# Optimization experiments

Measured on AMD Instinct MI355X. Metric: run time of the kernel, lower is better.

The kernel has to match this reference:

```python
import jax, jax.numpy as jnp
import numpy as np

B, T, N, D, INTER, KS = 8, 12, 325, 64, 16, 3
BN_EPS = 1e-5
LN_EPS = 1e-5


def _stx(x):
    # [B,T,N,D] -> edge-pad time, unfold window 3 -> [B,T,3N,D] (window-major like torch reshape)
    xp = jnp.concatenate([x[:, :1], x, x[:, -1:]], axis=1)          # [B,T+2,N,D]
    w = jnp.stack([xp[:, i:i + T] for i in range(3)], axis=2)        # [B,T,3,N,D]
    return w.reshape(x.shape[0], T, 3 * N, x.shape[-1])


def _conv1x1(y, W, b):
    # y: [B,C,T,N], W: [O,C], b: [O]
    return jnp.einsum('bctn,oc->botn', y, W) + b[None, :, None, None]


def _bn_eval(y, g, b):
    # BatchNorm2d eval with running mean 0 / var 1
    return y * (g / jnp.sqrt(1.0 + BN_EPS))[None, :, None, None] + b[None, :, None, None]


def setup_inputs() -> dict:
    key = jax.random.key(0)
    ks = jax.random.split(key, 32)
    inp = {}
    inp['x'] = jax.random.normal(ks[0], (B, T, N, D), jnp.float32)
    inp['gso'] = jax.random.normal(ks[1], (B, N, N), jnp.float32) * 0.05
    inp['geo_mask'] = jax.random.bernoulli(ks[2], 0.5, (N, N))
    s = 1.0 / np.sqrt(D)
    inp['Wq'] = jax.random.normal(ks[3], (D, D), jnp.float32) * s
    inp['Wk'] = jax.random.normal(ks[4], (D, D), jnp.float32) * s
    inp['Wv'] = jax.random.normal(ks[5], (D, D), jnp.float32) * s
    inp['cheb_w'] = jax.random.normal(ks[6], (KS, D, D), jnp.float32) * s
    inp['p_t12'] = jax.random.normal(ks[7], (N,), jnp.float32)
    inp['p_t21'] = jax.random.normal(ks[8], (N,), jnp.float32)
    inp['p_t23'] = jax.random.normal(ks[9], (N,), jnp.float32)
    inp['p_t32'] = jax.random.normal(ks[10], (N,), jnp.float32)
    inp['ln_g'] = jnp.ones((D,), jnp.float32)
    inp['ln_b'] = jnp.zeros((D,), jnp.float32)
    si = 1.0 / np.sqrt(INTER)
    for pfx, kk in (('l', 11), ('g', 17)):
        inp[pfx + '_w1'] = jax.random.normal(ks[kk], (INTER, D), jnp.float32) * s
        inp[pfx + '_b1'] = jax.random.normal(ks[kk + 1], (INTER,), jnp.float32) * s
        inp[pfx + '_g1'] = jnp.ones((INTER,), jnp.float32)
        inp[pfx + '_be1'] = jnp.zeros((INTER,), jnp.float32)
        inp[pfx + '_w2'] = jax.random.normal(ks[kk + 2], (D, INTER), jnp.float32) * si
        inp[pfx + '_b2'] = jax.random.normal(ks[kk + 3], (D,), jnp.float32) * si
        inp[pfx + '_g2'] = jnp.ones((D,), jnp.float32)
        inp[pfx + '_be2'] = jnp.zeros((D,), jnp.float32)
    return inp


def _forward(x, gso, geo_mask, Wq, Wk, Wv, cheb_w, p_t12, p_t21, p_t23, p_t32,
             ln_g, ln_b,
             l_w1, l_b1, l_g1, l_be1, l_w2, l_b2, l_g2, l_be2,
             g_w1, g_b1, g_g1, g_be1, g_w2, g_b2, g_g2, g_be2):
    M = 3 * N
    stX = _stx(x)                                                    # [B,T,M,D]

    # ---- DSTFormer: masked spatiotemporal attention (no scaling, per source) ----
    q = jnp.einsum('btmd,od->btmo', stX, Wq)
    k = jnp.einsum('btmd,od->btmo', stX, Wk)
    v = jnp.einsum('btmd,od->btmo', stX, Wv)
    attn = jnp.einsum('btmo,btno->btmn', q, k)                       # [B,T,M,M]
    eye = jnp.eye(N, dtype=bool)
    uneye = ~eye
    tru = jnp.ones((N, N), dtype=bool)
    big_mask = jnp.block([[geo_mask, uneye, tru],
                          [uneye, geo_mask, uneye],
                          [tru, uneye, geo_mask]])                   # [M,M]
    attn = jnp.where(big_mask, -jnp.inf, attn)
    p = jax.nn.softmax(attn, axis=-1)
    sem = jnp.einsum('btmn,btno->btmo', p, v)                        # [B,T,M,D]
    # faithful to torch: transpose(2,3) then reshape(B,T,M,-1) (mixes layout)
    y = jnp.swapaxes(sem, 2, 3).reshape(B, T, M, D)
    attn_out = y.reshape(B, T, 3, N, D)[:, :, 1]                     # [B,T,N,D]

    # ---- DSTGCN: Chebyshev conv on assembled [B,3N,3N] shift operator ----
    Z = jnp.zeros((B, N, N), x.dtype)
    dg = lambda vv: jnp.broadcast_to(jnp.diag(vv), (B, N, N))
    row0 = jnp.concatenate([gso, dg(p_t21), Z], axis=2)
    row1 = jnp.concatenate([dg(p_t12), gso, dg(p_t32)], axis=2)
    row2 = jnp.concatenate([Z, dg(p_t23), gso], axis=2)
    L = jnp.concatenate([row0, row1, row2], axis=1)                  # [B,M,M]
    xs = [stX, jnp.einsum('bhi,btij->bthj', L, stX)]
    for kk in range(2, KS):
        xs.append(jnp.einsum('bhi,btij->bthj', 2.0 * L, xs[kk - 1]) - xs[kk - 2])
    xk = jnp.stack(xs, axis=2)                                       # [B,T,KS,M,D]
    h = jnp.einsum('btkhi,kij->bthj', xk, cheb_w)                    # [B,T,M,D]
    h = jnp.transpose(h, (0, 3, 1, 2)).reshape(B, D, T, 3, N)[:, :, :, 1, :]  # [B,D,T,N]
    h = jnp.transpose(h, (0, 2, 3, 1))                               # [B,T,N,D]
    mu = h.mean(-1, keepdims=True)
    var = ((h - mu) ** 2).mean(-1, keepdims=True)
    gcn_out = (h - mu) / jnp.sqrt(var + LN_EPS) * ln_g + ln_b

    # ---- AFF fusion on channel-first maps ----
    xc = jnp.transpose(attn_out, (0, 3, 1, 2))                       # [B,D,T,N]
    rc = jnp.transpose(gcn_out, (0, 3, 1, 2))
    xa = xc + rc
    zl = jax.nn.relu(_bn_eval(_conv1x1(xa, l_w1, l_b1), l_g1, l_be1))
    xl = _bn_eval(_conv1x1(zl, l_w2, l_b2), l_g2, l_be2)
    m = xa.mean((2, 3), keepdims=True)
    zg = jax.nn.relu(_bn_eval(_conv1x1(m, g_w1, g_b1), g_g1, g_be1))
    xg = _bn_eval(_conv1x1(zg, g_w2, g_b2), g_g2, g_be2)
    wei = jax.nn.sigmoid(xl + xg)
    out = 2.0 * xc * wei + 2.0 * rc * (1.0 - wei)
    return jnp.transpose(out, (0, 2, 3, 1))                          # [B,T,N,D]


def reference(x, gso, geo_mask, Wq, Wk, Wv, cheb_w, p_t12, p_t21, p_t23, p_t32,
              ln_g, ln_b,
              l_w1, l_b1, l_g1, l_be1, l_w2, l_b2, l_g2, l_be2,
              g_w1, g_b1, g_g1, g_be1, g_w2, g_b2, g_g2, g_be2):
    return _forward(x, gso, geo_mask, Wq, Wk, Wv, cheb_w, p_t12, p_t21, p_t23, p_t32,
                    ln_g, ln_b,
                    l_w1, l_b1, l_g1, l_be1, l_w2, l_b2, l_g2, l_be2,
                    g_w1, g_b1, g_g1, g_be1, g_w2, g_b2, g_g2, g_be2)
```

## Files before the change

### kernel.cpp

```cpp
#include <hip/hip_runtime.h>
#include <math.h>

constexpr int TT = 12;
constexpr int NN = 325;
constexpr int MM = 975;
constexpr int DD = 64;
constexpr long SZ = 96L * MM * DD;
constexpr int GSTR = 352;
constexpr int MBSTR = 48;
constexpr int VTS = 22528;
constexpr float BN_EPS_ = 1e-5f;
constexpr float LN_EPS_ = 1e-5f;

constexpr long WS_MASKB = 0;
constexpr long WS_GSOB  = WS_MASKB + 4096;
constexpr long WS_STXB  = WS_GSOB + 457600;
constexpr long WS_QB    = WS_STXB + SZ / 2;
constexpr long WS_KB    = WS_QB + SZ / 2;
constexpr long WS_VB    = WS_KB + SZ / 2;
constexpr long WS_VT    = WS_VB + SZ / 2;
constexpr long WS_SEMH  = WS_VT + 3244032;
constexpr long WS_T2B   = WS_SEMH + SZ / 2;
constexpr long WS_MBD   = WS_T2B + 998400;

typedef _Float16 half8 __attribute__((ext_vector_type(8)));
typedef __attribute__((ext_vector_type(4))) float f32x4;

static __device__ inline unsigned short f2h(float f) {
  _Float16 h = (_Float16)f;
  return __builtin_bit_cast(unsigned short, h);
}
static __device__ inline float h2f(unsigned short s) {
  return (float)__builtin_bit_cast(_Float16, s);
}

__global__ __launch_bounds__(256) void k_maskprep(const unsigned char* __restrict__ raw,
                                                  unsigned char* __restrict__ outm) {
  bool is_u8 = false;
  for (int i = 0; i < 256; ++i) {
    if (raw[4 * i + 1]) { is_u8 = true; break; }
  }
  int idx = blockIdx.x * 256 + threadIdx.x;
  if (idx >= NN * MBSTR) return;
  int n = idx / MBSTR, jb = idx - n * MBSTR;
  unsigned char v = 0;
  for (int k = 0; k < 8; ++k) {
    int col = jb * 8 + k;
    bool m = true;
    if (col < NN) {
      int f = n * NN + col;
      m = is_u8 ? (raw[f] != 0) : (((const int*)raw)[f] != 0);
    }
    v |= (unsigned char)(m ? 1 : 0) << k;
  }
  outm[idx] = v;
}

__global__ __launch_bounds__(256) void k_gsoprep(const float* __restrict__ gso,
                                                 unsigned short* __restrict__ gsoB) {
  int idx = blockIdx.x * 256 + threadIdx.x;
  int b = idx / (NN * GSTR);
  int rem = idx - b * (NN * GSTR);
  int r = rem / GSTR, j = rem - r * GSTR;
  gsoB[idx] = (j < NN) ? f2h(gso[(long)b * NN * NN + r * NN + j]) : (unsigned short)0;
}

__global__ __launch_bounds__(256) void k_stx(const float* __restrict__ x,
                                             unsigned short* __restrict__ stXb) {
  int idx = blockIdx.x * 256 + threadIdx.x;
  int d = idx & 63;
  int m = (idx >> 6) % MM;
  int bt = idx / (MM * DD);
  int b = bt / TT, t = bt - b * TT;
  int w = m / NN, n = m - w * NN;
  int st = t + w - 1;
  st = st < 0 ? 0 : (st > TT - 1 ? TT - 1 : st);
  stXb[idx] = f2h(x[(((b * TT + st) * NN + n) << 6) + d]);
}

__global__ __launch_bounds__(256) void k_qkv_mfma(const unsigned short* __restrict__ stXb,
                                                  const float* __restrict__ Wq,
                                                  const float* __restrict__ Wk,
                                                  const float* __restrict__ Wv,
                                                  unsigned short* __restrict__ qb,
                                                  unsigned short* __restrict__ kb,
                                                  unsigned short* __restrict__ vb) {
  __shared__ alignas(16) unsigned short sX[128 * 72];
  __shared__ alignas(16) unsigned short sW[64 * 72];
  const float* W = blockIdx.y == 0 ? Wq : (blockIdx.y == 1 ? Wk : Wv);
  unsigned short* outb = blockIdx.y == 0 ? qb : (blockIdx.y == 1 ? kb : vb);
  int tid = threadIdx.x;
  long r0 = (long)blockIdx.x * 128;
  for (int u = 0; u < 4; ++u) {
    int idx = tid + 256 * u;
    int row = idx >> 3, c8 = idx & 7;
    long rg = r0 + row; if (rg > 93599) rg = 93599;
    *(uint4*)&sX[row * 72 + c8 * 8] = *(const uint4*)&stXb[rg * 64 + c8 * 8];
  }
  for (int u = 0; u < 16; ++u) {
    int f = tid + 256 * u;
    int o = f >> 6, d = f & 63;
    sW[o * 72 + d] = f2h(W[f]);
  }
  __syncthreads();
  int lane = tid & 63;
  int wv = __builtin_amdgcn_readfirstlane(tid >> 6);
  int lr = lane & 15, lg = lane >> 4;
  f32x4 zero4 = {0.f, 0.f, 0.f, 0.f};
  f32x4 acc[2][4];
#pragma unroll
  for (int rt = 0; rt < 2; ++rt)
#pragma unroll
    for (int c = 0; c < 4; ++c) acc[rt][c] = zero4;
#pragma unroll
  for (int kk = 0; kk < 2; ++kk) {
    half8 a0 = *(const half8*)&sX[(32 * wv + lr) * 72 + kk * 32 + lg * 8];
    half8 a1 = *(const half8*)&sX[(32 * wv + 16 + lr) * 72 + kk * 32 + lg * 8];
#pragma unroll
    for (int c = 0; c < 4; ++c) {
      half8 b = *(const half8*)&sW[(16 * c + lr) * 72 + kk * 32 + lg * 8];
      acc[0][c] = __builtin_amdgcn_mfma_f32_16x16x32_f16(a0, b, acc[0][c], 0, 0, 0);
      acc[1][c] = __builtin_amdgcn_mfma_f32_16x16x32_f16(a1, b, acc[1][c], 0, 0, 0);
    }
  }
  __syncthreads();
#pragma unroll
  for (int rt = 0; rt < 2; ++rt)
#pragma unroll
    for (int c = 0; c < 4; ++c)
#pragma unroll
      for (int e = 0; e < 4; ++e) {
        int row = 32 * wv + 16 * rt + lg * 4 + e;
        int col = 16 * c + lr;
        sX[row * 64 + col] = f2h(acc[rt][c][e]);
      }
  __syncthreads();
  for (int u = 0; u < 4; ++u) {
    int idx = tid + 256 * u;
    int row = idx >> 3, c8 = idx & 7;
    long rg = r0 + row;
    if (rg < 93600)
      *(uint4*)&outb[rg * 64 + c8 * 8] = *(const uint4*)&sX[row * 64 + c8 * 8];
  }
}

__global__ __launch_bounds__(256) void k_vT(const unsigned short* __restrict__ vb,
                                            unsigned short* __restrict__ vbT) {
  __shared__ alignas(16) unsigned short T[128 * 72];
  int seg = blockIdx.x;
  int ck = blockIdx.y;
  int tid = threadIdx.x;
  long base = (long)seg * NN * 64;
  int k0 = ck * 128;
  for (int u = 0; u < 4; ++u) {
    int idx = tid + 256 * u;
    int row = idx >> 3, c8 = idx & 7;
    int kg = k0 + row;
    uint4 v;
    if (kg < NN) v = *(const uint4*)&vb[base + (long)kg * 64 + c8 * 8];
    else { v.x = 0; v.y = 0; v.z = 0; v.w = 0; }
    *(uint4*)&T[row * 72 + c8 * 8] = v;
  }
  __syncthreads();
  int d = tid & 63, k8 = tid >> 6;
  for (int it = 0; it < 4; ++it) {
    int klocal = (it * 4 + k8) * 8;
    if (k0 + klocal < 352) {
      unsigned short tmp[8];
#pragma unroll
      for (int j = 0; j < 8; ++j) tmp[j] = T[(klocal + j) * 72 + d];
      *(uint4*)&vbT[(long)seg * VTS + (long)d * 352 + k0 + klocal] = *(const uint4*)tmp;
    }
  }
}

__global__ __launch_bounds__(256, 3) void k_attn(const unsigned short* __restrict__ qb,
                                                 const unsigned short* __restrict__ kb,
                                                 const unsigned short* __restrict__ vb,
                                                 const unsigned short* __restrict__ vbT,
                                                 const unsigned char* __restrict__ maskb,
                                                 unsigned short* __restrict__ semh) {
  __shared__ unsigned char Mb[64 * MBSTR];
  __shared__ alignas(16) unsigned short Ptr4[4 * 16 * 40];
  int seg = blockIdx.x;
  int bt = seg / 3, w = seg - bt * 3;
  int rt = blockIdx.y;
  long segbase = (long)seg * NN * 64;
  int tid = threadIdx.x;
  if (tid < 192) {
    int r = tid / 3, c16 = tid - (tid / 3) * 3;
    int rg = rt * 64 + r; if (rg > NN - 1) rg = NN - 1;
    *(uint4*)&Mb[r * MBSTR + c16 * 16] = *(const uint4*)&maskb[(long)rg * MBSTR + c16 * 16];
  }
  __syncthreads();
  int lane = tid & 63;
  int wv = __builtin_amdgcn_readfirstlane(tid >> 6);
  int lr = lane & 15, lg = lane >> 4;
  f32x4 zero4 = {0.f, 0.f, 0.f, 0.f};
  f32x4 acc[21];
#pragma unroll
  for (int ct = 0; ct < 21; ++ct) acc[ct] = zero4;
  f32x4 dA = zero4, dB = zero4;
  int arow = rt * 64 + 16 * wv + lr; if (arow > NN - 1) arow = NN - 1;
  long abase = segbase + (long)arow * 64;
  int nl_f = arow;
  long pAaddr = ((long)bt * MM + ((w == 1) ? nl_f : NN + nl_f)) * 64;
  long pBaddr = ((long)bt * MM + 2 * NN + nl_f) * 64;
#pragma unroll
  for (int kk = 0; kk < 2; ++kk) {
    half8 a = *(const half8*)&qb[abase + kk * 32 + lg * 8];
#pragma unroll
    for (int ct = 0; ct < 21; ++ct) {
      int brow = 16 * ct + lr; if (brow > NN - 1) brow = NN - 1;
      half8 b = *(const half8*)&kb[segbase + (long)brow * 64 + kk * 32 + lg * 8];
      acc[ct] = __builtin_amdgcn_mfma_f32_16x16x32_f16(a, b, acc[ct], 0, 0, 0);
    }
    half8 bA = *(const half8*)&kb[pAaddr + kk * 32 + lg * 8];
    dA = __builtin_amdgcn_mfma_f32_16x16x32_f16(a, bA, dA, 0, 0, 0);
    if (w == 1) {
      half8 bB = *(const half8*)&kb[pBaddr + kk * 32 + lg * 8];
      dB = __builtin_amdgcn_mfma_f32_16x16x32_f16(a, bB, dB, 0, 0, 0);
    }
  }
  float da_[4], db_[4];
#pragma unroll
  for (int e = 0; e < 4; ++e) {
    int src = lg * 20 + e;
    da_[e] = __shfl(dA[e], src);
    db_[e] = (w == 1) ? __shfl(dB[e], src) : -INFINITY;
  }
  float mx[4] = {-INFINITY, -INFINITY, -INFINITY, -INFINITY};
  unsigned mw[4];
#pragma unroll
  for (int ct = 0; ct < 21; ++ct) {
    if ((ct & 1) == 0) {
#pragma unroll
      for (int e = 0; e < 4; ++e) {
        int rl = 16 * wv + lg * 4 + e;
        mw[e] = *(const unsigned*)&Mb[rl * MBSTR + (ct >> 1) * 4];
      }
    }
    int sh = 16 * (ct & 1) + lr;
#pragma unroll
    for (int e = 0; e < 4; ++e) {
      bool masked = (mw[e] >> sh) & 1;
      float s = masked ? -INFINITY : acc[ct][e];
      acc[ct][e] = s;
      mx[e] = fmaxf(mx[e], s);
    }
  }
#pragma unroll
  for (int e = 0; e < 4; ++e)
    for (int m = 1; m < 16; m <<= 1) mx[e] = fmaxf(mx[e], __shfl_xor(mx[e], m));
  float gm[4], ea[4], eb[4], sum[4], inv[4];
#pragma unroll
  for (int e = 0; e < 4; ++e) {
    gm[e] = fmaxf(mx[e], da_[e]);
    if (w == 1) gm[e] = fmaxf(gm[e], db_[e]);
    sum[e] = 0.f;
  }
#pragma unroll
  for (int ct = 0; ct < 21; ++ct)
#pragma unroll
    for (int e = 0; e < 4; ++e) {
      float s = acc[ct][e];
      float p = (s > -1e37f) ? __expf(s - gm[e]) : 0.f;
      acc[ct][e] = p;
      sum[e] += p;
    }
#pragma unroll
  for (int e = 0; e < 4; ++e) {
    for (int m = 1; m < 16; m <<= 1) sum[e] += __shfl_xor(sum[e], m);
    ea[e] = __expf(da_[e] - gm[e]);
    eb[e] = (w == 1) ? __expf(db_[e] - gm[e]) : 0.f;
    sum[e] += ea[e] + eb[e];
    inv[e] = 1.f / sum[e];
  }
  unsigned short* Ptr = Ptr4 + wv * 640;
  long vtbase = (long)seg * VTS;
  f32x4 oacc[4];
#pragma unroll
  for (int c = 0; c < 4; ++c) oacc[c] = zero4;
#pragma unroll
  for (int ck = 0; ck < 11; ++ck) {
#pragma unroll
    for (int t = 0; t < 2; ++t) {
      int ct = 2 * ck + t;
#pragma unroll
      for (int e = 0; e < 4; ++e) {
        float pv = (ct < 21) ? acc[ct][e] * inv[e] : 0.f;
        Ptr[(lg * 4 + e) * 40 + t * 16 + lr] = f2h(pv);
      }
    }
    half8 a = *(const half8*)&Ptr[lr * 40 + lg * 8];
#pragma unroll
    for (int c = 0; c < 4; ++c) {
      half8 b = *(const half8*)&vbT[vtbase + (long)(16 * c + lr) * 352 + ck * 32 + lg * 8];
      oacc[c] = __builtin_amdgcn_mfma_f32_16x16x32_f16(a, b, oacc[c], 0, 0, 0);
    }
  }
#pragma unroll
  for (int c = 0; c < 4; ++c)
#pragma unroll
    for (int e = 0; e < 4; ++e) {
      int n = rt * 64 + 16 * wv + lg * 4 + e;
      int col = 16 * c + lr;
      if (n < NN) {
        float val = oacc[c][e];
        int partA = (w == 1) ? n : NN + n;
        val += ea[e] * inv[e] * h2f(vb[((long)bt * MM + partA) * 64 + col]);
        if (w == 1)
          val += eb[e] * inv[e] * h2f(vb[((long)bt * MM + 2 * NN + n) * 64 + col]);
        semh[((long)bt * MM + (long)w * NN + n) * 64 + col] = f2h(val);
      }
    }
}

__global__ __launch_bounds__(256) void k_xs1_mfma(const unsigned short* __restrict__ gsoB,
                                                  const unsigned short* __restrict__ stXb,
                                                  const float* __restrict__ pt12,
                                                  const float* __restrict__ pt21,
                                                  const float* __restrict__ pt23,
                                                  const float* __restrict__ pt32,
                                                  unsigned short* __restrict__ xs1b) {
  __shared__ alignas(16) unsigned short Al[128 * 40];
  __shared__ alignas(16) unsigned short Bt[64 * 40];
  int btw = blockIdx.x;
  int bt = btw / 3, w = btw - bt * 3;
  int b = bt / TT;
  int rt_blk = blockIdx.y;
  const unsigned short* A = gsoB + (long)b * NN * GSTR;
  long vbase = (long)bt * MM + (long)w * NN;
  int tid = threadIdx.x;
  int lane = tid & 63;
  int wv = __builtin_amdgcn_readfirstlane(tid >> 6);
  int lr = lane & 15, lg = lane >> 4;
  f32x4 zero4 = {0.f, 0.f, 0.f, 0.f};
  f32x4 acc[2][4];
#pragma unroll
  for (int rt = 0; rt < 2; ++rt)
#pragma unroll
    for (int c = 0; c < 4; ++c) acc[rt][c] = zero4;
  for (int kb_ = 0; kb_ < 352; kb_ += 32) {
    __syncthreads();
    for (int u = 0; u < 2; ++u) {
      int idx = tid + 256 * u;
      int row = idx >> 2, c8 = idx & 3;
      int rr = rt_blk * 128 + row; if (rr > NN - 1) rr = NN - 1;
      *(uint4*)&Al[row * 40 + c8 * 8] = *(const uint4*)&A[(long)rr * GSTR + kb_ + c8 * 8];
    }
    for (int u = 0; u < 2; ++u) {
      int idx = tid + 256 * u;
      int k = idx >> 4, c4 = idx & 15;
      int kg = kb_ + k;
#pragma unroll
      for (int j = 0; j < 4; ++j) {
        int d = c4 + 16 * j;
        unsigned short val = (kg < NN) ? stXb[(vbase + kg) * 64 + d] : (unsigned short)0;
        Bt[d * 40 + k] = val;
      }
    }
    __syncthreads();
    half8 a0 = *(const half8*)&Al[(32 * wv + lr) * 40 + lg * 8];
    half8 a1 = *(const half8*)&Al[(32 * wv + 16 + lr) * 40 + lg * 8];
#pragma unroll
    for (int c = 0; c < 4; ++c) {
      half8 b_ = *(const half8*)&Bt[(16 * c + lr) * 40 + lg * 8];
      acc[0][c] = __builtin_amdgcn_mfma_f32_16x16x32_f16(a0, b_, acc[0][c], 0, 0, 0);
      acc[1][c] = __builtin_amdgcn_mfma_f32_16x16x32_f16(a1, b_, acc[1][c], 0, 0, 0);
    }
  }
  long btM = (long)bt * MM;
#pragma unroll
  for (int rt = 0; rt < 2; ++rt)
#pragma unroll
    for (int c = 0; c < 4; ++c)
#pragma unroll
      for (int e = 0; e < 4; ++e) {
        int n = rt_blk * 128 + 32 * wv + 16 * rt + lg * 4 + e;
        int col = 16 * c + lr;
        if (n < NN) {
          float val = acc[rt][c][e];
          if (w == 0) {
            val += pt21[n] * h2f(stXb[(btM + NN + n) * 64 + col]);
          } else if (w == 1) {
            val += pt12[n] * h2f(stXb[(btM + n) * 64 + col])
                 + pt32[n] * h2f(stXb[(btM + 2 * NN + n) * 64 + col]);
          } else {
            val += pt23[n] * h2f(stXb[(btM + NN + n) * 64 + col]);
          }
          xs1b[(btM + (long)w * NN + n) * 64 + col] = f2h(val);
        }
      }
}

__global__ __launch_bounds__(256) void k_t2_mfma(const unsigned short* __restrict__ gsoB,
                                                 const unsigned short* __restrict__ xs1b,
                                                 const unsigned short* __restrict__ stXb,
                                                 const float* __restrict__ pt12,
                                                 const float* __restrict__ pt32,
                                                 unsigned short* __restrict__ t2b) {
  __shared__ alignas(16) unsigned short Al[128 * 40];
  __shared__ alignas(16) unsigned short Bt[64 * 40];
  int bt = blockIdx.x;
  int b = bt / TT;
  int rt_blk = blockIdx.y;
  const unsigned short* A = gsoB + (long)b * NN * GSTR;
  long vbase = (long)bt * MM + NN;
  int tid = threadIdx.x;
  int lane = tid & 63;
  int wv = __builtin_amdgcn_readfirstlane(tid >> 6);
  int lr = lane & 15, lg = lane >> 4;
  f32x4 zero4 = {0.f, 0.f, 0.f, 0.f};
  f32x4 acc[2][4];
#pragma unroll
  for (int rt = 0; rt < 2; ++rt)
#pragma unroll
    for (int c = 0; c < 4; ++c) acc[rt][c] = zero4;
  for (int kb_ = 0; kb_ < 352; kb_ += 32) {
    __syncthreads();
    for (int u = 0; u < 2; ++u) {
      int idx = tid + 256 * u;
      int row = idx >> 2, c8 = idx & 3;
      int rr = rt_blk * 128 + row; if (rr > NN - 1) rr = NN - 1;
      *(uint4*)&Al[row * 40 + c8 * 8] = *(const uint4*)&A[(long)rr * GSTR + kb_ + c8 * 8];
    }
    for (int u = 0; u < 2; ++u) {
      int idx = tid + 256 * u;
      int k = idx >> 4, c4 = idx & 15;
      int kg = kb_ + k;
#pragma unroll
      for (int j = 0; j < 4; ++j) {
        int d = c4 + 16 * j;
        unsigned short val = (kg < NN) ? xs1b[(vbase + kg) * 64 + d] : (unsigned short)0;
        Bt[d * 40 + k] = val;
      }
    }
    __syncthreads();
    half8 a0 = *(const half8*)&Al[(32 * wv + lr) * 40 + lg * 8];
    half8 a1 = *(const half8*)&Al[(32 * wv + 16 + lr) * 40 + lg * 8];
#pragma unroll
    for (int c = 0; c < 4; ++c) {
      half8 b_ = *(const half8*)&Bt[(16 * c + lr) * 40 + lg * 8];
      acc[0][c] = __builtin_amdgcn_mfma_f32_16x16x32_f16(a0, b_, acc[0][c], 0, 0, 0);
      acc[1][c] = __builtin_amdgcn_mfma_f32_16x16x32_f16(a1, b_, acc[1][c], 0, 0, 0);
    }
  }
  long btM = (long)bt * MM;
#pragma unroll
  for (int rt = 0; rt < 2; ++rt)
#pragma unroll
    for (int c = 0; c < 4; ++c)
#pragma unroll
      for (int e = 0; e < 4; ++e) {
        int n = rt_blk * 128 + 32 * wv + 16 * rt + lg * 4 + e;
        int col = 16 * c + lr;
        if (n < NN) {
          float val = 2.f * (pt12[n] * h2f(xs1b[(btM + n) * 64 + col])
                             + acc[rt][c][e]
                             + pt32[n] * h2f(xs1b[(btM + 2 * NN + n) * 64 + col]))
                      - h2f(stXb[(btM + NN + n) * 64 + col]);
          t2b[((long)bt * NN + n) * 64 + col] = f2h(val);
        }
      }
}

__global__ __launch_bounds__(256) void k_cheb_mfma(const unsigned short* __restrict__ stXb,
                                                   const unsigned short* __restrict__ xs1b,
                                                   const unsigned short* __restrict__ t2b,
                                                   const float* __restrict__ cw,
                                                   const float* __restrict__ lng,
                                                   const float* __restrict__ lnb,
                                                   float* __restrict__ gcn) {
  __shared__ alignas(16) unsigned short Bt[64 * 200];
  __shared__ alignas(16) unsigned short Al[128 * 40];
  int tid = threadIdx.x;
  for (int u = 0; u < 48; ++u) {
    int f = tid + 256 * u;
    int K = f >> 6, j = f & 63;
    Bt[j * 200 + K] = f2h(cw[f]);
  }
  int lane = tid & 63;
  int wv = __builtin_amdgcn_readfirstlane(tid >> 6);
  int lr = lane & 15, lg = lane >> 4;
  long grow0 = (long)blockIdx.x * 128;
  f32x4 zero4 = {0.f, 0.f, 0.f, 0.f};
  f32x4 acc[2][4];
#pragma unroll
  for (int rt = 0; rt < 2; ++rt)
#pragma unroll
    for (int c = 0; c < 4; ++c) acc[rt][c] = zero4;
  for (int ch = 0; ch < 6; ++ch) {
    const unsigned short* src = ch < 2 ? stXb : (ch < 4 ? xs1b : t2b);
    int koff = (ch & 1) * 32;
    __syncthreads();
    for (int u = 0; u < 2; ++u) {
      int idx = tid + 256 * u;
      int row = idx >> 2, c8 = idx & 3;
      long gr = grow0 + row; if (gr > 31199) gr = 31199;
      int bt = (int)(gr / NN), n = (int)(gr - (long)bt * NN);
      long sbase = (ch < 4) ? ((long)bt * MM + NN + n) * 64 : gr * 64;
      *(uint4*)&Al[row * 40 + c8 * 8] = *(const uint4*)&src[sbase + koff + c8 * 8];
    }
    __syncthreads();
    half8 a0 = *(const half8*)&Al[(32 * wv + lr) * 40 + lg * 8];
    half8 a1 = *(const half8*)&Al[(32 * wv + 16 + lr) * 40 + lg * 8];
#pragma unroll
    for (int c = 0; c < 4; ++c) {
      half8 b = *(const half8*)&Bt[(16 * c + lr) * 200 + ch * 32 + lg * 8];
      acc[0][c] = __builtin_amdgcn_mfma_f32_16x16x32_f16(a0, b, acc[0][c], 0, 0, 0);
      acc[1][c] = __builtin_amdgcn_mfma_f32_16x16x32_f16(a1, b, acc[1][c], 0, 0, 0);
    }
  }
  float lngv[4], lnbv[4];
#pragma unroll
  for (int c = 0; c < 4; ++c) { lngv[c] = lng[16 * c + lr]; lnbv[c] = lnb[16 * c + lr]; }
#pragma unroll
  for (int rt = 0; rt < 2; ++rt)
#pragma unroll
    for (int e = 0; e < 4; ++e) {
      float s = acc[rt][0][e] + acc[rt][1][e] + acc[rt][2][e] + acc[rt][3][e];
      for (int m = 1; m < 16; m <<= 1) s += __shfl_xor(s, m);
      float mu = s * (1.f / 64.f);
      float q = 0.f;
#pragma unroll
      for (int c = 0; c < 4; ++c) { float d = acc[rt][c][e] - mu; q += d * d; }
      for (int m = 1; m < 16; m <<= 1) q += __shfl_xor(q, m);
      float rstd = rsqrtf(q * (1.f / 64.f) + LN_EPS_);
      long gr = grow0 + 32 * wv + 16 * rt + lg * 4 + e;
      if (gr < 31200) {
#pragma unroll
        for (int c = 0; c < 4; ++c)
          gcn[gr * 64 + 16 * c + lr] = (acc[rt][c][e] - mu) * rstd * lngv[c] + lnbv[c];
      }
    }
}

__global__ __launch_bounds__(256) void k_mean(const unsigned short* __restrict__ semh,
                                              const float* __restrict__ gcn,
                                              float* __restrict__ mbd) {
  __shared__ float red[4][64];
  int bt = blockIdx.x;
  int b = bt / TT;
  int d = threadIdx.x & 63, g = threadIdx.x >> 6;
  float s = 0.f;
  for (int n = g; n < NN; n += 4) {
    int f = (NN + n) * 64 + d;
    int mm = f % MM, ii = f / MM;
    float a = h2f(semh[((long)bt * MM + mm) * 64 + ii]);
    float r = gcn[((long)bt * NN + n) * 64 + d];
    s += a + r;
  }
  red[g][d] = s;
  __syncthreads();
  if (threadIdx.x < 64) {
    float v = red[0][d] + red[1][d] + red[2][d] + red[3][d];
    atomicAdd(&mbd[b * 64 + d], v);
  }
}

__global__ __launch_bounds__(64) void k_glob(const float* __restrict__ mbd,
                                             const float* __restrict__ w1,
                                             const float* __restrict__ b1,
                                             const float* __restrict__ g1,
                                             const float* __restrict__ be1,
                                             const float* __restrict__ w2,
                                             const float* __restrict__ b2,
                                             const float* __restrict__ g2,
                                             const float* __restrict__ be2,
                                             float* __restrict__ xg) {
  __shared__ float ml[64];
  __shared__ float zg[16];
  int b = blockIdx.x, d = threadIdx.x;
  ml[d] = mbd[b * 64 + d] * (1.f / 3900.f);
  __syncthreads();
  float rb = rsqrtf(1.f + BN_EPS_);
  if (d < 16) {
    float a = b1[d];
    for (int i = 0; i < 64; ++i) a += w1[d * 64 + i] * ml[i];
    a = a * (g1[d] * rb) + be1[d];
    zg[d] = a > 0.f ? a : 0.f;
  }
  __syncthreads();
  float a = b2[d];
  for (int i = 0; i < 16; ++i) a += w2[d * 16 + i] * zg[i];
  xg[b * 64 + d] = a * (g2[d] * rb) + be2[d];
}

__global__ __launch_bounds__(256) void k_final(const unsigned short* __restrict__ semh,
                                               const float* __restrict__ gcn,
                                               const float* __restrict__ xg,
                                               const float* __restrict__ w1,
                                               const float* __restrict__ b1,
                                               const float* __restrict__ g1,
                                               const float* __restrict__ be1,
                                               const float* __restrict__ w2,
                                               const float* __restrict__ b2,
                                               const float* __restrict__ g2,
                                               const float* __restrict__ be2,
                                               float* __restrict__ out) {
  __shared__ float w1l[16][65];
  __shared__ float w2l[64][17];
  __shared__ float xal[4][64];
  __shared__ float zll[4][16];
  int tid = threadIdx.x;
  for (int u = 0; u < 4; ++u) {
    int f = tid + 256 * u;
    w1l[f >> 6][f & 63] = w1[f];
    w2l[f >> 4][f & 15] = w2[f];
  }
  int lane = tid & 63, wv = tid >> 6;
  long row = (long)blockIdx.x * 4 + wv;
  int bt = (int)(row / NN);
  int n = (int)(row - (long)bt * NN);
  int b = bt / TT;
  int f = (NN + n) * 64 + lane;
  int mm = f % MM, ii = f / MM;
  float a = h2f(semh[((long)bt * MM + mm) * 64 + ii]);
  float r = gcn[row * DD + lane];
  float xa = a + r;
  xal[wv][lane] = xa;
  __syncthreads();
  float rb = rsqrtf(1.f + BN_EPS_);
  if (lane < 16) {
    float acc = b1[lane];
#pragma unroll 8
    for (int i = 0; i < 64; ++i) acc += w1l[lane][i] * xal[wv][i];
    acc = acc * (g1[lane] * rb) + be1[lane];
    zll[wv][lane] = acc > 0.f ? acc : 0.f;
  }
  __syncthreads();
  float acc = b2[lane];
#pragma unroll
  for (int i = 0; i < 16; ++i) acc += w2l[lane][i] * zll[wv][i];
  float xl = acc * (g2[lane] * rb) + be2[lane];
  float wei = 1.f / (1.f + __expf(-(xl + xg[b * 64 + lane])));
  out[row * DD + lane] = 2.f * a * wei + 2.f * r * (1.f - wei);
}

extern "C" void kernel_launch(void* const* d_in, const int* in_sizes, int n_in,
                              void* d_out, int out_size, void* d_ws, size_t ws_size,
                              hipStream_t stream) {
  const float* x    = (const float*)d_in[0];
  const float* gso  = (const float*)d_in[1];
  const unsigned char* mask_raw = (const unsigned char*)d_in[2];
  const float* Wq   = (const float*)d_in[3];
  const float* Wk   = (const float*)d_in[4];
  const float* Wv   = (const float*)d_in[5];
  const float* chw  = (const float*)d_in[6];
  const float* pt12 = (const float*)d_in[7];
  const float* pt21 = (const float*)d_in[8];
  const float* pt23 = (const float*)d_in[9];
  const float* pt32 = (const float*)d_in[10];
  const float* lng  = (const float*)d_in[11];
  const float* lnb  = (const float*)d_in[12];
  const float* l_w1 = (const float*)d_in[13];
  const float* l_b1 = (const float*)d_in[14];
  const float* l_g1 = (const float*)d_in[15];
  const float* l_be1= (const float*)d_in[16];
  const float* l_w2 = (const float*)d_in[17];
  const float* l_b2 = (const float*)d_in[18];
  const float* l_g2 = (const float*)d_in[19];
  const float* l_be2= (const float*)d_in[20];
  const float* g_w1 = (const float*)d_in[21];
  const float* g_b1 = (const float*)d_in[22];
  const float* g_g1 = (const float*)d_in[23];
  const float* g_be1= (const float*)d_in[24];
  const float* g_w2 = (const float*)d_in[25];
  const float* g_b2 = (const float*)d_in[26];
  const float* g_g2 = (const float*)d_in[27];
  const float* g_be2= (const float*)d_in[28];

  float* base = (float*)d_ws;
  unsigned char* maskb = (unsigned char*)d_ws;
  unsigned short* gsoB = (unsigned short*)(base + WS_GSOB);
  unsigned short* stXb = (unsigned short*)(base + WS_STXB);
  unsigned short* qb   = (unsigned short*)(base + WS_QB);
  unsigned short* kb   = (unsigned short*)(base + WS_KB);
  unsigned short* vb   = (unsigned short*)(base + WS_VB);
  unsigned short* vbT  = (unsigned short*)(base + WS_VT);
  unsigned short* semh = (unsigned short*)(base + WS_SEMH);
  unsigned short* t2b  = (unsigned short*)(base + WS_T2B);

  unsigned short* xs1b = vb;
  float* gcn = (float*)qb;
  float* mbd = base + WS_MBD;
  float* xg  = mbd + 512;

  k_maskprep<<<(NN * MBSTR + 255) / 256, 256, 0, stream>>>(mask_raw, maskb);
  k_gsoprep<<<3575, 256, 0, stream>>>(gso, gsoB);
  k_stx<<<23400, 256, 0, stream>>>(x, stXb);
  {
    dim3 g(732, 3);
    k_qkv_mfma<<<g, 256, 0, stream>>>(stXb, Wq, Wk, Wv, qb, kb, vb);
  }
  {
    dim3 gv(288, 3);
    k_vT<<<gv, 256, 0, stream>>>(vb, vbT);
  }
  {
    dim3 ga(288, 6);
    k_attn<<<ga, 256, 0, stream>>>(qb, kb, vb, vbT, maskb, semh);
  }
  {
    dim3 g(288, 3);
    k_xs1_mfma<<<g, 256, 0, stream>>>(gsoB, stXb, pt12, pt21, pt23, pt32, xs1b);
  }
  {
    dim3 g(96, 3);
    k_t2_mfma<<<g, 256, 0, stream>>>(gsoB, xs1b, stXb, pt12, pt32, t2b);
  }
  k_cheb_mfma<<<244, 256, 0, stream>>>(stXb, xs1b, t2b, chw, lng, lnb, gcn);
  hipMemsetAsync(mbd, 0, 1024 * sizeof(float), stream);
  k_mean<<<96, 256, 0, stream>>>(semh, gcn, mbd);
  k_glob<<<8, 64, 0, stream>>>(mbd, g_w1, g_b1, g_g1, g_be1, g_w2, g_b2, g_g2, g_be2, xg);
  k_final<<<7800, 256, 0, stream>>>(semh, gcn, xg,
                                    l_w1, l_b1, l_g1, l_be1,
                                    l_w2, l_b2, l_g2, l_be2,
                                    (float*)d_out);
}
```

Measured before the change: 370.1 us.

## Split attention into single-wave blocks with swizzled block order

Restructures the attention kernel from 256-thread blocks covering 64 query rows into 64-thread blocks covering 16 rows. Blocks are remapped with an XCD-style swizzle. The shared-memory mask staging and its barrier are dropped, and each lane now reads the mask bytes from global memory directly. The aim is to remove the padding waste (325 rows in 6×64 tiles) and the block-level sync, and to improve occupancy and L2 locality. In exchange the block count is four times higher and mask loads go through global memory.

New measurement: 359.2 us. 1.03x faster.

```diff
diff --git a/kernel.cpp b/kernel.cpp
--- a/kernel.cpp
+++ b/kernel.cpp
@@ -174,38 +174,30 @@
   }
 }
 
-__global__ __launch_bounds__(256, 3) void k_attn(const unsigned short* __restrict__ qb,
-                                                 const unsigned short* __restrict__ kb,
-                                                 const unsigned short* __restrict__ vb,
-                                                 const unsigned short* __restrict__ vbT,
-                                                 const unsigned char* __restrict__ maskb,
-                                                 unsigned short* __restrict__ semh) {
-  __shared__ unsigned char Mb[64 * MBSTR];
-  __shared__ alignas(16) unsigned short Ptr4[4 * 16 * 40];
-  int seg = blockIdx.x;
+__global__ __launch_bounds__(64, 3) void k_attn(const unsigned short* __restrict__ qb,
+                                                const unsigned short* __restrict__ kb,
+                                                const unsigned short* __restrict__ vb,
+                                                const unsigned short* __restrict__ vbT,
+                                                const unsigned char* __restrict__ maskb,
+                                                unsigned short* __restrict__ semh) {
+  __shared__ alignas(16) unsigned short Ptr[16 * 40];
+  int bid = blockIdx.x;
+  int swz = (bid & 7) * 756 + (bid >> 3);
+  int seg = swz / 21, rti = swz - seg * 21;
   int bt = seg / 3, w = seg - bt * 3;
-  int rt = blockIdx.y;
+  int n0 = rti * 16;
   long segbase = (long)seg * NN * 64;
-  int tid = threadIdx.x;
-  if (tid < 192) {
-    int r = tid / 3, c16 = tid - (tid / 3) * 3;
-    int rg = rt * 64 + r; if (rg > NN - 1) rg = NN - 1;
-    *(uint4*)&Mb[r * MBSTR + c16 * 16] = *(const uint4*)&maskb[(long)rg * MBSTR + c16 * 16];
-  }
-  __syncthreads();
-  int lane = tid & 63;
-  int wv = __builtin_amdgcn_readfirstlane(tid >> 6);
+  int lane = threadIdx.x;
   int lr = lane & 15, lg = lane >> 4;
   f32x4 zero4 = {0.f, 0.f, 0.f, 0.f};
   f32x4 acc[21];
 #pragma unroll
   for (int ct = 0; ct < 21; ++ct) acc[ct] = zero4;
   f32x4 dA = zero4, dB = zero4;
-  int arow = rt * 64 + 16 * wv + lr; if (arow > NN - 1) arow = NN - 1;
+  int arow = n0 + lr; if (arow > NN - 1) arow = NN - 1;
   long abase = segbase + (long)arow * 64;
-  int nl_f = arow;
-  long pAaddr = ((long)bt * MM + ((w == 1) ? nl_f : NN + nl_f)) * 64;
-  long pBaddr = ((long)bt * MM + 2 * NN + nl_f) * 64;
+  long pAaddr = ((long)bt * MM + ((w == 1) ? arow : NN + arow)) * 64;
+  long pBaddr = ((long)bt * MM + 2 * NN + arow) * 64;
 #pragma unroll
   for (int kk = 0; kk < 2; ++kk) {
     half8 a = *(const half8*)&qb[abase + kk * 32 + lg * 8];
@@ -229,16 +221,20 @@
     da_[e] = __shfl(dA[e], src);
     db_[e] = (w == 1) ? __shfl(dB[e], src) : -INFINITY;
   }
+  int rl[4];
+#pragma unroll
+  for (int e = 0; e < 4; ++e) {
+    int r = n0 + lg * 4 + e; if (r > NN - 1) r = NN - 1;
+    rl[e] = r;
+  }
   float mx[4] = {-INFINITY, -INFINITY, -INFINITY, -INFINITY};
   unsigned mw[4];
 #pragma unroll
   for (int ct = 0; ct < 21; ++ct) {
     if ((ct & 1) == 0) {
 #pragma unroll
-      for (int e = 0; e < 4; ++e) {
-        int rl = 16 * wv + lg * 4 + e;
-        mw[e] = *(const unsigned*)&Mb[rl * MBSTR + (ct >> 1) * 4];
-      }
+      for (int e = 0; e < 4; ++e)
+        mw[e] = *(const unsigned*)&maskb[(long)rl[e] * MBSTR + (ct >> 1) * 4];
     }
     int sh = 16 * (ct & 1) + lr;
 #pragma unroll
@@ -276,7 +272,6 @@
     sum[e] += ea[e] + eb[e];
     inv[e] = 1.f / sum[e];
   }
-  unsigned short* Ptr = Ptr4 + wv * 640;
   long vtbase = (long)seg * VTS;
   f32x4 oacc[4];
 #pragma unroll
@@ -303,7 +298,7 @@
   for (int c = 0; c < 4; ++c)
 #pragma unroll
     for (int e = 0; e < 4; ++e) {
-      int n = rt * 64 + 16 * wv + lg * 4 + e;
+      int n = n0 + lg * 4 + e;
       int col = 16 * c + lr;
       if (n < NN) {
         float val = oacc[c][e];
@@ -698,10 +693,7 @@
     dim3 gv(288, 3);
     k_vT<<<gv, 256, 0, stream>>>(vb, vbT);
   }
-  {
-    dim3 ga(288, 6);
-    k_attn<<<ga, 256, 0, stream>>>(qb, kb, vb, vbT, maskb, semh);
-  }
+  k_attn<<<6048, 64, 0, stream>>>(qb, kb, vb, vbT, maskb, semh);
   {
     dim3 g(288, 3);
     k_xs1_mfma<<<g, 256, 0, stream>>>(gsoB, stXb, pt12, pt21, pt23, pt32, xs1b);
```
